# Kernel optimization log

Measured on AMD Instinct MI355X. Metric: run time of the kernel, lower is better.

Reference implementation:

```python
import jax, jax.numpy as jnp
import numpy as np

N_ITERS = 32       # fixed round count; >> worst-case active-set rounds (each round clamps all violators)
NBIKES = 512.0     # global sum constraint C (env.nbikes)


def _project(y, lower, upper):
    """Active-set (water-filling) projection of one vector y onto
    {z : lower <= z <= upper, sum(z) = NBIKES}.
    phase 0: clamp to lower; phase 1: clamp to upper; phase 2: done.
    """
    def step(state, _):
        m, zc, C, phase = state              # m: 1.0 = unclamped; zc: clamped values
        mb = m > 0.5
        n_un = jnp.maximum(jnp.sum(m), 1.0)
        s = jnp.sum(jnp.where(mb, y, 0.0))
        z = y + (C - s) / n_un               # equal water-fill over unclamped set
        active = phase < 2
        viol = jnp.where(phase == 0, z < lower, z > upper) & mb & active
        cval = jnp.where(phase == 0, lower, upper)
        zc = jnp.where(viol, cval, zc)
        C = C - jnp.sum(jnp.where(viol, cval, 0.0))
        m = jnp.where(viol, 0.0, m)
        phase = jnp.where(active & ~jnp.any(viol), phase + 1, phase)
        return (m, zc, C, phase), None

    m0 = jnp.ones_like(y)
    zc0 = jnp.zeros_like(y)
    C0 = jnp.asarray(NBIKES, y.dtype)
    p0 = jnp.asarray(0, jnp.int32)
    (m, zc, C, _), _ = jax.lax.scan(step, (m0, zc0, C0, p0), None, length=N_ITERS)
    mb = m > 0.5
    n_un = jnp.maximum(jnp.sum(m), 1.0)
    s = jnp.sum(jnp.where(mb, y, 0.0))
    z = y + (C - s) / n_un
    return jnp.where(mb, z, zc)


def setup_inputs() -> dict:
    key = jax.random.key(0)
    k1, k2 = jax.random.split(key)
    B, N = 2048, 1024
    y = jax.random.normal(k1, (B, N), dtype=jnp.float32)
    upper = jax.random.uniform(k2, (N,), dtype=jnp.float32, minval=0.1, maxval=2.0)
    return {"y": y, "upper": upper}


def reference(y, upper):
    lower = jnp.zeros_like(upper)
    return jax.vmap(lambda yi: _project(yi, lower, upper))(y)
```

## Files before the change

### kernel.cpp

```cpp
#include <hip/hip_runtime.h>


#define N_COLS 1024
#define NBIKES 512.0f

__global__ __launch_bounds__(256) void proj_rows(
    const float* __restrict__ y,
    const float* __restrict__ upper,
    float* __restrict__ out,
    int B)
{
    const int lane = threadIdx.x & 63;
    const int wave = threadIdx.x >> 6;
    const int row  = (blockIdx.x << 2) + wave;
    if (row >= B) return;

    const float* yrow = y + (size_t)row * N_COLS;

    float4 yv[4], uv[4], zc[4];
#pragma unroll
    for (int j = 0; j < 4; ++j) {
        const int idx = (j << 8) + (lane << 2);
        yv[j] = *reinterpret_cast<const float4*>(yrow + idx);
        uv[j] = *reinterpret_cast<const float4*>(upper + idx);
        zc[j] = make_float4(0.f, 0.f, 0.f, 0.f);
    }

    unsigned mask = 0xFFFFu;
    float C = NBIKES;
    int phase = 0;

    for (int it = 0; it < 32 && phase < 2; ++it) {
        float n_un = 0.f, s = 0.f;
#pragma unroll
        for (int j = 0; j < 4; ++j) {
            const float* yp = reinterpret_cast<const float*>(&yv[j]);
#pragma unroll
            for (int k = 0; k < 4; ++k) {
                if ((mask >> ((j << 2) + k)) & 1u) { n_un += 1.f; s += yp[k]; }
            }
        }
#pragma unroll
        for (int off = 32; off >= 1; off >>= 1) {
            n_un += __shfl_xor(n_un, off, 64);
            s    += __shfl_xor(s,    off, 64);
        }
        const float t = (C - s) / fmaxf(n_un, 1.0f);

        bool lane_viol = false;
        float csum = 0.f;
#pragma unroll
        for (int j = 0; j < 4; ++j) {
            const float* yp = reinterpret_cast<const float*>(&yv[j]);
            const float* up = reinterpret_cast<const float*>(&uv[j]);
            float* zp = reinterpret_cast<float*>(&zc[j]);
#pragma unroll
            for (int k = 0; k < 4; ++k) {
                const int b = (j << 2) + k;
                if (!((mask >> b) & 1u)) continue;
                const float z = yp[k] + t;
                const bool v = (phase == 0) ? (z < 0.f) : (z > up[k]);
                if (v) {
                    const float cv = (phase == 0) ? 0.f : up[k];
                    zp[k]  = cv;
                    csum  += cv;
                    mask  &= ~(1u << b);
                    lane_viol = true;
                }
            }
        }

        if (phase == 1) {
#pragma unroll
            for (int off = 32; off >= 1; off >>= 1)
                csum += __shfl_xor(csum, off, 64);
            C -= csum;
        }
        if (!__any((int)lane_viol)) ++phase;
    }

    float n_un = 0.f, s = 0.f;
#pragma unroll
    for (int j = 0; j < 4; ++j) {
        const float* yp = reinterpret_cast<const float*>(&yv[j]);
#pragma unroll
        for (int k = 0; k < 4; ++k)
            if ((mask >> ((j << 2) + k)) & 1u) { n_un += 1.f; s += yp[k]; }
    }
#pragma unroll
    for (int off = 32; off >= 1; off >>= 1) {
        n_un += __shfl_xor(n_un, off, 64);
        s    += __shfl_xor(s,    off, 64);
    }
    const float t = (C - s) / fmaxf(n_un, 1.0f);

    float* orow = out + (size_t)row * N_COLS;
#pragma unroll
    for (int j = 0; j < 4; ++j) {
        const float* yp = reinterpret_cast<const float*>(&yv[j]);
        const float* zp = reinterpret_cast<const float*>(&zc[j]);
        float4 o;
        float* op = reinterpret_cast<float*>(&o);
#pragma unroll
        for (int k = 0; k < 4; ++k) {
            const int b = (j << 2) + k;
            op[k] = ((mask >> b) & 1u) ? (yp[k] + t) : zp[k];
        }
        *reinterpret_cast<float4*>(orow + (j << 8) + (lane << 2)) = o;
    }
}

extern "C" void kernel_launch(void* const* d_in, const int* in_sizes, int n_in,
                              void* d_out, int out_size, void* d_ws, size_t ws_size,
                              hipStream_t stream) {
    const float* yv    = (const float*)d_in[0];
    const float* upper = (const float*)d_in[1];
    float* out = (float*)d_out;
    const int B = in_sizes[0] / N_COLS;
    const int blocks = (B + 3) >> 2;
    proj_rows<<<blocks, 256, 0, stream>>>(yv, upper, out, B);
}
```

Before: 81.04 us.

## Track residual sum incrementally and use DPP wave reductions

Instead of recomputing the unclamped count and sum over all elements each round, the kernel computes the row sum once and then subtracts only the newly clamped elements' contributions, with one fused reduction per round. Clamped values are reconstructed at output from a bitmask rather than stored in registers. Wave reductions switch from shuffle-xor to DPP row operations plus readlane. This changes floating-point summation order, so results may differ slightly from the reference.

```diff
diff --git a/kernel.cpp b/kernel.cpp
--- a/kernel.cpp
+++ b/kernel.cpp
@@ -3,6 +3,21 @@
 
 #define N_COLS 1024
 #define NBIKES 512.0f
+
+#define DPP_ADD2(ctrl)                                                                         \
+    a += __int_as_float(__builtin_amdgcn_update_dpp(0, __float_as_int(a), (ctrl), 0xf, 0xf, true)); \
+    b += __int_as_float(__builtin_amdgcn_update_dpp(0, __float_as_int(b), (ctrl), 0xf, 0xf, true));
+
+__device__ __forceinline__ void wave_sum2(float& a, float& b) {
+    DPP_ADD2(0x111)
+    DPP_ADD2(0x112)
+    DPP_ADD2(0x114)
+    DPP_ADD2(0x118)
+    DPP_ADD2(0x142)
+    DPP_ADD2(0x143)
+    a = __int_as_float(__builtin_amdgcn_readlane(__float_as_int(a), 63));
+    b = __int_as_float(__builtin_amdgcn_readlane(__float_as_int(b), 63));
+}
 
 __global__ __launch_bounds__(256) void proj_rows(
     const float* __restrict__ y,
@@ -17,94 +32,84 @@
 
     const float* yrow = y + (size_t)row * N_COLS;
 
-    float4 yv[4], uv[4], zc[4];
+    float4 yv[4], uv[4];
 #pragma unroll
     for (int j = 0; j < 4; ++j) {
         const int idx = (j << 8) + (lane << 2);
         yv[j] = *reinterpret_cast<const float4*>(yrow + idx);
         uv[j] = *reinterpret_cast<const float4*>(upper + idx);
-        zc[j] = make_float4(0.f, 0.f, 0.f, 0.f);
     }
 
-    unsigned mask = 0xFFFFu;
-    float C = NBIKES;
+    float s_part = 0.f, zero = 0.f;
+#pragma unroll
+    for (int j = 0; j < 4; ++j) {
+        const float* yp = reinterpret_cast<const float*>(&yv[j]);
+#pragma unroll
+        for (int k = 0; k < 4; ++k) s_part += yp[k];
+    }
+    wave_sum2(s_part, zero);
+
+    float d = NBIKES - s_part;
+    float n = (float)N_COLS;
+    unsigned alive = 0xFFFFu;
+    unsigned hi    = 0u;
     int phase = 0;
 
     for (int it = 0; it < 32 && phase < 2; ++it) {
-        float n_un = 0.f, s = 0.f;
+        const float t = d / fmaxf(n, 1.0f);
+        float delta = 0.f;
+        float cnt   = 0.f;
+
+        if (phase == 0) {
 #pragma unroll
-        for (int j = 0; j < 4; ++j) {
-            const float* yp = reinterpret_cast<const float*>(&yv[j]);
+            for (int j = 0; j < 4; ++j) {
+                const float* yp = reinterpret_cast<const float*>(&yv[j]);
 #pragma unroll
-            for (int k = 0; k < 4; ++k) {
-                if ((mask >> ((j << 2) + k)) & 1u) { n_un += 1.f; s += yp[k]; }
+                for (int k = 0; k < 4; ++k) {
+                    const int b = (j << 2) + k;
+                    const bool v = ((alive >> b) & 1u) && (yp[k] + t < 0.f);
+                    if (v) { delta -= yp[k]; cnt += 1.f; alive &= ~(1u << b); }
+                }
             }
-        }
+        } else {
 #pragma unroll
-        for (int off = 32; off >= 1; off >>= 1) {
-            n_un += __shfl_xor(n_un, off, 64);
-            s    += __shfl_xor(s,    off, 64);
-        }
-        const float t = (C - s) / fmaxf(n_un, 1.0f);
-
-        bool lane_viol = false;
-        float csum = 0.f;
+            for (int j = 0; j < 4; ++j) {
+                const float* yp = reinterpret_cast<const float*>(&yv[j]);
+                const float* up = reinterpret_cast<const float*>(&uv[j]);
 #pragma unroll
-        for (int j = 0; j < 4; ++j) {
-            const float* yp = reinterpret_cast<const float*>(&yv[j]);
-            const float* up = reinterpret_cast<const float*>(&uv[j]);
-            float* zp = reinterpret_cast<float*>(&zc[j]);
-#pragma unroll
-            for (int k = 0; k < 4; ++k) {
-                const int b = (j << 2) + k;
-                if (!((mask >> b) & 1u)) continue;
-                const float z = yp[k] + t;
-                const bool v = (phase == 0) ? (z < 0.f) : (z > up[k]);
-                if (v) {
-                    const float cv = (phase == 0) ? 0.f : up[k];
-                    zp[k]  = cv;
-                    csum  += cv;
-                    mask  &= ~(1u << b);
-                    lane_viol = true;
+                for (int k = 0; k < 4; ++k) {
+                    const int b = (j << 2) + k;
+                    const bool v = ((alive >> b) & 1u) && (yp[k] + t > up[k]);
+                    if (v) {
+                        delta += up[k] - yp[k];
+                        cnt   += 1.f;
+                        alive &= ~(1u << b);
+                        hi    |= (1u << b);
+                    }
                 }
             }
         }
 
-        if (phase == 1) {
-#pragma unroll
-            for (int off = 32; off >= 1; off >>= 1)
-                csum += __shfl_xor(csum, off, 64);
-            C -= csum;
-        }
-        if (!__any((int)lane_viol)) ++phase;
+        wave_sum2(delta, cnt);
+        d -= delta;
+        n -= cnt;
+        if (cnt == 0.f) ++phase;
     }
 
-    float n_un = 0.f, s = 0.f;
-#pragma unroll
-    for (int j = 0; j < 4; ++j) {
-        const float* yp = reinterpret_cast<const float*>(&yv[j]);
-#pragma unroll
-        for (int k = 0; k < 4; ++k)
-            if ((mask >> ((j << 2) + k)) & 1u) { n_un += 1.f; s += yp[k]; }
-    }
-#pragma unroll
-    for (int off = 32; off >= 1; off >>= 1) {
-        n_un += __shfl_xor(n_un, off, 64);
-        s    += __shfl_xor(s,    off, 64);
-    }
-    const float t = (C - s) / fmaxf(n_un, 1.0f);
+    const float t = d / fmaxf(n, 1.0f);
 
     float* orow = out + (size_t)row * N_COLS;
 #pragma unroll
     for (int j = 0; j < 4; ++j) {
         const float* yp = reinterpret_cast<const float*>(&yv[j]);
-        const float* zp = reinterpret_cast<const float*>(&zc[j]);
+        const float* up = reinterpret_cast<const float*>(&uv[j]);
         float4 o;
         float* op = reinterpret_cast<float*>(&o);
 #pragma unroll
         for (int k = 0; k < 4; ++k) {
             const int b = (j << 2) + k;
-            op[k] = ((mask >> b) & 1u) ? (yp[k] + t) : zp[k];
+            op[k] = ((alive >> b) & 1u) ? (yp[k] + t)
+                   : (((hi >> b) & 1u) ? up[k] : 0.f);
         }
         *reinterpret_cast<float4*>(orow + (j << 8) + (lane << 2)) = o;
     }
```

Result: faster. 67.00 us (-17.3%).
